# Performance work log

Hardware: AMD Instinct MI355X
Metric: run time of the kernel (lower is better)

Reference implementation:

```python
import jax, jax.numpy as jnp
import numpy as np

B, D, L = 4, 256, 4096

def setup_inputs() -> dict:
    key = jax.random.key(0)
    k1, k2, k3 = jax.random.split(key, 3)
    query = jax.random.normal(k1, (B, D, L), dtype=jnp.float32)
    context = jax.random.normal(k2, (B, D, L), dtype=jnp.float32)
    W_in = jax.random.normal(k3, (D, D), dtype=jnp.float32) * 0.02
    b_in = jnp.zeros((D,), dtype=jnp.float32)
    return {"query": query, "context": context, "W_in": W_in, "b_in": b_in}

def reference(query, context, W_in, b_in):
    # inputs are [B, D, L]; module transposes to [B, L, D]
    q = jnp.transpose(query, (0, 2, 1))    # [B, O, D]
    c = jnp.transpose(context, (0, 2, 1))  # [B, Q, D]
    # 'general': linear_in applied to query only (torch Linear: x @ W^T + b)
    q = q @ W_in.T + b_in
    # unscaled Luong attention: QK^T -> softmax -> A V
    scores = jnp.einsum('bod,bqd->boq', q, c)          # [B, O, Q]
    weights = jax.nn.softmax(scores, axis=-1)          # [B, O, Q]
    out = jnp.einsum('boq,bqd->bod', weights, c)       # [B, O, D]
    return (out, weights)
```

## Files before the change

kernel.cpp:

```cpp
#include <hip/hip_runtime.h>


#define BATCH 4
#define DDIM  256
#define LSEQ  4096
#define TQ    64

typedef float    f32x4 __attribute__((ext_vector_type(4)));
typedef _Float16 f16x8 __attribute__((ext_vector_type(8)));
typedef _Float16 f16x4 __attribute__((ext_vector_type(4)));

__device__ __forceinline__ void gld16(const void* g, void* l) {
  __builtin_amdgcn_global_load_lds((const __attribute__((address_space(1))) void*)g,
                                   (__attribute__((address_space(3))) void*)l, 16, 0, 0);
}

__global__ __launch_bounds__(256) void transpose_cast(
    const float* __restrict__ q_in, const float* __restrict__ c_in,
    _Float16* __restrict__ q_out, _Float16* __restrict__ c_out)
{
  __shared__ float tile[64][68];
  const int which = blockIdx.z >> 2;
  const int b     = blockIdx.z & 3;
  const float* __restrict__ src = which ? c_in : q_in;
  _Float16* __restrict__ dst    = which ? c_out : q_out;
  const int l0 = blockIdx.x * 64, d0 = blockIdx.y * 64;
  const int tid = threadIdx.x;
  const int tr = tid >> 4, tc = (tid & 15) << 2;
#pragma unroll
  for (int i = 0; i < 4; ++i) {
    int d = tr + i * 16;
    f32x4 v = *(const f32x4*)(src + ((size_t)b * DDIM + d0 + d) * LSEQ + l0 + tc);
    *(f32x4*)&tile[d][tc] = v;
  }
  __syncthreads();
#pragma unroll
  for (int i = 0; i < 4; ++i) {
    int l = tr + i * 16;
    f16x4 h;
    h[0] = (_Float16)tile[tc + 0][l];
    h[1] = (_Float16)tile[tc + 1][l];
    h[2] = (_Float16)tile[tc + 2][l];
    h[3] = (_Float16)tile[tc + 3][l];
    *(f16x4*)(dst + ((size_t)b * LSEQ + l0 + l) * DDIM + d0 + tc) = h;
  }
}

__global__ __launch_bounds__(256) void wconv(const float* __restrict__ w,
                                             _Float16* __restrict__ w16) {
  int i = (blockIdx.x * 256 + threadIdx.x) * 4;
  f32x4 v = *(const f32x4*)(w + i);
  f16x4 h;
  h[0] = (_Float16)v[0]; h[1] = (_Float16)v[1];
  h[2] = (_Float16)v[2]; h[3] = (_Float16)v[3];
  *(f16x4*)(w16 + i) = h;
}

__global__ __launch_bounds__(256) void castD(const float* __restrict__ c_in,
                                             _Float16* __restrict__ cD16) {
  size_t i = ((size_t)blockIdx.x * 256 + threadIdx.x) * 8;
  f32x4 a = *(const f32x4*)(c_in + i);
  f32x4 b = *(const f32x4*)(c_in + i + 4);
  f16x8 h;
  h[0] = (_Float16)a[0]; h[1] = (_Float16)a[1];
  h[2] = (_Float16)a[2]; h[3] = (_Float16)a[3];
  h[4] = (_Float16)b[0]; h[5] = (_Float16)b[1];
  h[6] = (_Float16)b[2]; h[7] = (_Float16)b[3];
  *(f16x8*)(cD16 + i) = h;
}

__global__ __launch_bounds__(256) void linear_q(
    const _Float16* __restrict__ qT16, const _Float16* __restrict__ W16,
    const float* __restrict__ bias, _Float16* __restrict__ qw16)
{
  const int tid = threadIdx.x;
  const int wv = tid >> 6, ln = tid & 63, g = ln >> 4, c16 = ln & 15;
  const size_t r0 = (size_t)blockIdx.x * 64 + wv * 16;

  f16x8 qa[8];
  const _Float16* qrow = qT16 + (r0 + c16) * DDIM + g * 8;
#pragma unroll
  for (int kk = 0; kk < 8; ++kk) qa[kk] = *(const f16x8*)(qrow + kk * 32);

  f32x4 acc[16];
#pragma unroll
  for (int n = 0; n < 16; ++n) acc[n] = f32x4{0.f, 0.f, 0.f, 0.f};

#pragma unroll 2
  for (int kk = 0; kk < 8; ++kk) {
#pragma unroll
    for (int n = 0; n < 16; ++n) {
      f16x8 bf = *(const f16x8*)(W16 + (n * 16 + c16) * DDIM + kk * 32 + g * 8);
      acc[n] = __builtin_amdgcn_mfma_f32_16x16x32_f16(qa[kk], bf, acc[n], 0, 0, 0);
    }
  }
#pragma unroll
  for (int n = 0; n < 16; ++n) {
    float bb = bias[n * 16 + c16];
#pragma unroll
    for (int r = 0; r < 4; ++r)
      qw16[(r0 + 4 * g + r) * DDIM + n * 16 + c16] = (_Float16)(acc[n][r] + bb);
  }
}

__global__ __launch_bounds__(256) void attn_main(
    const _Float16* __restrict__ qw16,
    const _Float16* __restrict__ cT16,
    const _Float16* __restrict__ cD16,
    float* __restrict__ outp,
    float* __restrict__ wgt)
{
  __shared__ __align__(16) char smem[2][65536];
  __shared__ __align__(16) char wbuf[8192];

  const int tid = threadIdx.x;
  const int wv  = tid >> 6;
  const int ln  = tid & 63;
  const int g   = ln >> 4;
  const int c16 = ln & 15;

  const int lin   = blockIdx.y * 64 + blockIdx.x;
  const int b     = (lin & 7) >> 1;
  const int otile = ((lin >> 3) << 1) | (lin & 1);
  const int o0    = otile * 64;
  const int bo    = b * LSEQ + o0;

  const _Float16* __restrict__ cbase = cT16 + (size_t)b * LSEQ * DDIM;
  const _Float16* __restrict__ cDb   = cD16 + (size_t)b * DDIM * LSEQ;

  f16x8 qa[8];
  {
    const _Float16* qrow = qw16 + ((size_t)bo + wv * 16 + c16) * DDIM + g * 8;
#pragma unroll
    for (int kk = 0; kk < 8; ++kk) qa[kk] = *(const f16x8*)(qrow + kk * 32);
  }

  auto issueA = [&](int q0s, int p) {
#pragma unroll
    for (int i = 0; i < 8; ++i) {
      unsigned x  = (unsigned)(wv * 8192 + i * 1024 + ln * 16);
      unsigned q  = x >> 9;
      unsigned db = (x & 511u) ^ ((q & 7u) << 4);
      gld16(cbase + (size_t)(q0s + q) * DDIM + (db >> 1),
            &smem[p][wv * 8192 + i * 1024]);
    }
  };
  auto issueC2 = [&](int q0s, int p) {
#pragma unroll
    for (int i = 0; i < 8; ++i) {
      unsigned x  = (unsigned)(wv * 8192 + i * 1024 + ln * 16);
      unsigned d  = x >> 7;
      unsigned qb = (x & 127u) ^ ((d & 7u) << 4);
      gld16(cDb + (size_t)d * LSEQ + q0s + (qb >> 1),
            &smem[p][32768 + wv * 8192 + i * 1024]);
    }
  };

  auto scores = [&](int p, f32x4 sa[4]) {
    const char* cl = smem[p];
#pragma unroll
    for (int qf = 0; qf < 4; ++qf) sa[qf] = f32x4{0.f, 0.f, 0.f, 0.f};
#pragma unroll
    for (int kk = 0; kk < 8; ++kk) {
#pragma unroll
      for (int qf = 0; qf < 4; ++qf) {
        unsigned off = (unsigned)(((qf * 16 + c16) * 512 + kk * 64 + g * 16)) ^
                       ((unsigned)(c16 & 7) << 4);
        f16x8 bf = *(const f16x8*)(cl + off);
        sa[qf] = __builtin_amdgcn_mfma_f32_16x16x32_f16(qa[kk], bf, sa[qf], 0, 0, 0);
      }
    }
  };

  float lsum[4] = {0.f, 0.f, 0.f, 0.f};
  int p = 0;
  issueA(0, 0);
  for (int t = 0; t < LSEQ / TQ; ++t) {
    asm volatile("s_waitcnt vmcnt(0)" ::: "memory");
    __builtin_amdgcn_s_barrier();
    if (t < LSEQ / TQ - 1) {
      issueA((t + 1) * TQ, p ^ 1);
    } else {
      issueA(0, p ^ 1);
      issueC2(0, p ^ 1);
    }
    __builtin_amdgcn_sched_barrier(0);
    f32x4 sa[4];
    scores(p, sa);
#pragma unroll
    for (int qf = 0; qf < 4; ++qf)
#pragma unroll
      for (int r = 0; r < 4; ++r) lsum[r] += __expf(sa[qf][r]);
    p ^= 1;
  }

  float invl[4];
#pragma unroll
  for (int r = 0; r < 4; ++r) {
    float v = lsum[r];
    v += __shfl_xor(v, 1);
    v += __shfl_xor(v, 2);
    v += __shfl_xor(v, 4);
    v += __shfl_xor(v, 8);
    invl[r] = 1.0f / v;
  }

  f32x4 oacc[4][4];
#pragma unroll
  for (int m = 0; m < 4; ++m)
#pragma unroll
    for (int nf = 0; nf < 4; ++nf) oacc[m][nf] = f32x4{0.f, 0.f, 0.f, 0.f};

  for (int t = 0; t < LSEQ / TQ; ++t) {
    if (t == 0) asm volatile("s_waitcnt vmcnt(0)" ::: "memory");
    else        asm volatile("s_waitcnt vmcnt(16)" ::: "memory");
    __builtin_amdgcn_s_barrier();
    if (t < LSEQ / TQ - 1) {
      issueA((t + 1) * TQ, p ^ 1);
      issueC2((t + 1) * TQ, p ^ 1);
    }
    __builtin_amdgcn_sched_barrier(0);

    const int q0 = t * TQ;
    f32x4 sa[4];
    scores(p, sa);

#pragma unroll
    for (int qf = 0; qf < 4; ++qf) {
#pragma unroll
      for (int r = 0; r < 4; ++r) {
        float w = __expf(sa[qf][r]) * invl[r];
        wgt[(size_t)(bo + wv * 16 + 4 * g + r) * LSEQ + (q0 + qf * 16 + c16)] = w;
        unsigned wb = (unsigned)((wv * 16 + 4 * g + r) * 128 + (qf * 16 + c16) * 2) ^
                      ((unsigned)((4 * g + r) & 7) << 4);
        *(_Float16*)(wbuf + wb) = (_Float16)w;
      }
    }
    asm volatile("s_waitcnt lgkmcnt(0)" ::: "memory");
    __builtin_amdgcn_s_barrier();
    __builtin_amdgcn_sched_barrier(0);

    const char* cl2 = smem[p] + 32768;
#pragma unroll
    for (int kq = 0; kq < 2; ++kq) {
      f16x8 wa[4], bv[4];
#pragma unroll
      for (int m = 0; m < 4; ++m) {
        unsigned off = (unsigned)((m * 16 + c16) * 128 + kq * 64 + g * 16) ^
                       ((unsigned)(c16 & 7) << 4);
        wa[m] = *(const f16x8*)(wbuf + off);
      }
#pragma unroll
      for (int nf = 0; nf < 4; ++nf) {
        unsigned off = (unsigned)((wv * 64 + nf * 16 + c16) * 128 + kq * 64 + g * 16) ^
                       ((unsigned)(c16 & 7) << 4);
        bv[nf] = *(const f16x8*)(cl2 + off);
      }
#pragma unroll
      for (int m = 0; m < 4; ++m)
#pragma unroll
        for (int nf = 0; nf < 4; ++nf)
          oacc[m][nf] =
              __builtin_amdgcn_mfma_f32_16x16x32_f16(wa[m], bv[nf], oacc[m][nf], 0, 0, 0);
    }
    p ^= 1;
  }

#pragma unroll
  for (int m = 0; m < 4; ++m)
#pragma unroll
    for (int nf = 0; nf < 4; ++nf)
#pragma unroll
      for (int r = 0; r < 4; ++r)
        outp[(size_t)(bo + m * 16 + 4 * g + r) * DDIM + wv * 64 + nf * 16 + c16] =
            oacc[m][nf][r];
}

extern "C" void kernel_launch(void* const* d_in, const int* in_sizes, int n_in,
                              void* d_out, int out_size, void* d_ws, size_t ws_size,
                              hipStream_t stream) {
  const float* query   = (const float*)d_in[0];
  const float* context = (const float*)d_in[1];
  const float* W_in    = (const float*)d_in[2];
  const float* b_in    = (const float*)d_in[3];

  float* outp = (float*)d_out;
  float* wgt  = outp + (size_t)BATCH * LSEQ * DDIM;

  const size_t NELEM = (size_t)BATCH * LSEQ * DDIM;
  _Float16* qT16 = (_Float16*)d_ws;
  _Float16* cT16 = qT16 + NELEM;
  _Float16* qw16 = cT16 + NELEM;
  _Float16* W16  = qw16 + NELEM;
  _Float16* cD16 = qT16;

  transpose_cast<<<dim3(LSEQ / 64, DDIM / 64, 2 * BATCH), 256, 0, stream>>>(
      query, context, qT16, cT16);
  wconv<<<(DDIM * DDIM) / 1024, 256, 0, stream>>>(W_in, W16);
  linear_q<<<(BATCH * LSEQ) / 64, 256, 0, stream>>>(qT16, W16, b_in, qw16);
  castD<<<(int)(NELEM / 2048), 256, 0, stream>>>(context, cD16);
  attn_main<<<dim3(64, BATCH), 256, 0, stream>>>(qw16, cT16, cD16, outp, wgt);
}
```

Baseline: 316.5 us.

## Split attention work across 8 waves per block with cross-wave reductions

Doubles the attn_main block to 512 threads. Each pair of waves now shares a 16-row query slice: in the score pass they split the 64-key tile into two 32-key halves, and in the A·V pass they split the K dimension. Row sums and partial output accumulators are combined through shared memory. The goal is more latency hiding and more MFMA issue parallelism, since only 256 blocks cover 256 CUs. In exchange it adds the reductions, an extra barrier, and more register pressure from the 512-thread launch bound.

```diff
diff --git a/kernel.cpp b/kernel.cpp
--- a/kernel.cpp
+++ b/kernel.cpp
@@ -103,7 +103,7 @@
   }
 }
 
-__global__ __launch_bounds__(256) void attn_main(
+__global__ __launch_bounds__(512) void attn_main(
     const _Float16* __restrict__ qw16,
     const _Float16* __restrict__ cT16,
     const _Float16* __restrict__ cD16,
@@ -112,9 +112,12 @@
 {
   __shared__ __align__(16) char smem[2][65536];
   __shared__ __align__(16) char wbuf[8192];
+  __shared__ float redbuf[2][64];
 
   const int tid = threadIdx.x;
   const int wv  = tid >> 6;
+  const int rw  = wv >> 1;
+  const int h   = wv & 1;
   const int ln  = tid & 63;
   const int g   = ln >> 4;
   const int c16 = ln & 15;
@@ -130,41 +133,41 @@
 
   f16x8 qa[8];
   {
-    const _Float16* qrow = qw16 + ((size_t)bo + wv * 16 + c16) * DDIM + g * 8;
+    const _Float16* qrow = qw16 + ((size_t)bo + rw * 16 + c16) * DDIM + g * 8;
 #pragma unroll
     for (int kk = 0; kk < 8; ++kk) qa[kk] = *(const f16x8*)(qrow + kk * 32);
   }
 
   auto issueA = [&](int q0s, int p) {
 #pragma unroll
-    for (int i = 0; i < 8; ++i) {
-      unsigned x  = (unsigned)(wv * 8192 + i * 1024 + ln * 16);
+    for (int i = 0; i < 4; ++i) {
+      unsigned x  = (unsigned)(wv * 4096 + i * 1024 + ln * 16);
       unsigned q  = x >> 9;
       unsigned db = (x & 511u) ^ ((q & 7u) << 4);
       gld16(cbase + (size_t)(q0s + q) * DDIM + (db >> 1),
-            &smem[p][wv * 8192 + i * 1024]);
+            &smem[p][wv * 4096 + i * 1024]);
     }
   };
   auto issueC2 = [&](int q0s, int p) {
 #pragma unroll
-    for (int i = 0; i < 8; ++i) {
-      unsigned x  = (unsigned)(wv * 8192 + i * 1024 + ln * 16);
+    for (int i = 0; i < 4; ++i) {
+      unsigned x  = (unsigned)(wv * 4096 + i * 1024 + ln * 16);
       unsigned d  = x >> 7;
       unsigned qb = (x & 127u) ^ ((d & 7u) << 4);
       gld16(cDb + (size_t)d * LSEQ + q0s + (qb >> 1),
-            &smem[p][32768 + wv * 8192 + i * 1024]);
+            &smem[p][32768 + wv * 4096 + i * 1024]);
     }
   };
 
-  auto scores = [&](int p, f32x4 sa[4]) {
+  auto scores = [&](int p, f32x4 sa[2]) {
     const char* cl = smem[p];
 #pragma unroll
-    for (int qf = 0; qf < 4; ++qf) sa[qf] = f32x4{0.f, 0.f, 0.f, 0.f};
+    for (int qf = 0; qf < 2; ++qf) sa[qf] = f32x4{0.f, 0.f, 0.f, 0.f};
 #pragma unroll
     for (int kk = 0; kk < 8; ++kk) {
 #pragma unroll
-      for (int qf = 0; qf < 4; ++qf) {
-        unsigned off = (unsigned)(((qf * 16 + c16) * 512 + kk * 64 + g * 16)) ^
+      for (int qf = 0; qf < 2; ++qf) {
+        unsigned off = (unsigned)(((h * 32 + qf * 16 + c16) * 512 + kk * 64 + g * 16)) ^
                        ((unsigned)(c16 & 7) << 4);
         f16x8 bf = *(const f16x8*)(cl + off);
         sa[qf] = __builtin_amdgcn_mfma_f32_16x16x32_f16(qa[kk], bf, sa[qf], 0, 0, 0);
@@ -185,16 +188,13 @@
       issueC2(0, p ^ 1);
     }
     __builtin_amdgcn_sched_barrier(0);
-    f32x4 sa[4];
+    f32x4 sa[2];
     scores(p, sa);
 #pragma unroll
-    for (int qf = 0; qf < 4; ++qf)
-#pragma unroll
-      for (int r = 0; r < 4; ++r) lsum[r] += __expf(sa[qf][r]);
+    for (int r = 0; r < 4; ++r) lsum[r] += __expf(sa[0][r]) + __expf(sa[1][r]);
     p ^= 1;
   }
 
-  float invl[4];
 #pragma unroll
   for (int r = 0; r < 4; ++r) {
     float v = lsum[r];
@@ -202,8 +202,17 @@
     v += __shfl_xor(v, 2);
     v += __shfl_xor(v, 4);
     v += __shfl_xor(v, 8);
-    invl[r] = 1.0f / v;
-  }
+    lsum[r] = v;
+  }
+  if (c16 == 0) {
+#pragma unroll
+    for (int r = 0; r < 4; ++r) redbuf[h][rw * 16 + 4 * g + r] = lsum[r];
+  }
+  __syncthreads();
+  float invl[4];
+#pragma unroll
+  for (int r = 0; r < 4; ++r)
+    invl[r] = 1.0f / (redbuf[0][rw * 16 + 4 * g + r] + redbuf[1][rw * 16 + 4 * g + r]);
 
   f32x4 oacc[4][4];
 #pragma unroll
@@ -213,7 +222,7 @@
 
   for (int t = 0; t < LSEQ / TQ; ++t) {
     if (t == 0) asm volatile("s_waitcnt vmcnt(0)" ::: "memory");
-    else        asm volatile("s_waitcnt vmcnt(16)" ::: "memory");
+    else        asm volatile("s_waitcnt vmcnt(8)" ::: "memory");
     __builtin_amdgcn_s_barrier();
     if (t < LSEQ / TQ - 1) {
       issueA((t + 1) * TQ, p ^ 1);
@@ -222,16 +231,18 @@
     __builtin_amdgcn_sched_barrier(0);
 
     const int q0 = t * TQ;
-    f32x4 sa[4];
+    f32x4 sa[2];
     scores(p, sa);
 
 #pragma unroll
-    for (int qf = 0; qf < 4; ++qf) {
+    for (int qf = 0; qf < 2; ++qf) {
 #pragma unroll
       for (int r = 0; r < 4; ++r) {
         float w = __expf(sa[qf][r]) * invl[r];
-        wgt[(size_t)(bo + wv * 16 + 4 * g + r) * LSEQ + (q0 + qf * 16 + c16)] = w;
-        unsigned wb = (unsigned)((wv * 16 + 4 * g + r) * 128 + (qf * 16 + c16) * 2) ^
+        int row = rw * 16 + 4 * g + r;
+        int col = h * 32 + qf * 16 + c16;
+        wgt[(size_t)(bo + row) * LSEQ + (q0 + col)] = w;
+        unsigned wb = (unsigned)(row * 128 + col * 2) ^
                       ((unsigned)((4 * g + r) & 7) << 4);
         *(_Float16*)(wbuf + wb) = (_Float16)w;
       }
@@ -241,18 +252,17 @@
     __builtin_amdgcn_sched_barrier(0);
 
     const char* cl2 = smem[p] + 32768;
-#pragma unroll
-    for (int kq = 0; kq < 2; ++kq) {
+    {
       f16x8 wa[4], bv[4];
 #pragma unroll
       for (int m = 0; m < 4; ++m) {
-        unsigned off = (unsigned)((m * 16 + c16) * 128 + kq * 64 + g * 16) ^
+        unsigned off = (unsigned)((m * 16 + c16) * 128 + h * 64 + g * 16) ^
                        ((unsigned)(c16 & 7) << 4);
         wa[m] = *(const f16x8*)(wbuf + off);
       }
 #pragma unroll
       for (int nf = 0; nf < 4; ++nf) {
-        unsigned off = (unsigned)((wv * 64 + nf * 16 + c16) * 128 + kq * 64 + g * 16) ^
+        unsigned off = (unsigned)((rw * 64 + nf * 16 + c16) * 128 + h * 64 + g * 16) ^
                        ((unsigned)(c16 & 7) << 4);
         bv[nf] = *(const f16x8*)(cl2 + off);
       }
@@ -266,14 +276,26 @@
     p ^= 1;
   }
 
-#pragma unroll
-  for (int m = 0; m < 4; ++m)
-#pragma unroll
-    for (int nf = 0; nf < 4; ++nf)
-#pragma unroll
-      for (int r = 0; r < 4; ++r)
-        outp[(size_t)(bo + m * 16 + 4 * g + r) * DDIM + wv * 64 + nf * 16 + c16] =
-            oacc[m][nf][r];
+  if (h == 1) {
+#pragma unroll
+    for (int m = 0; m < 4; ++m)
+#pragma unroll
+      for (int nf = 0; nf < 4; ++nf)
+        *(f32x4*)(smem[0] + rw * 16384 + (m * 4 + nf) * 1024 + ln * 16) = oacc[m][nf];
+  }
+  __syncthreads();
+  if (h == 0) {
+#pragma unroll
+    for (int m = 0; m < 4; ++m)
+#pragma unroll
+      for (int nf = 0; nf < 4; ++nf) {
+        f32x4 o2 = *(const f32x4*)(smem[0] + rw * 16384 + (m * 4 + nf) * 1024 + ln * 16);
+        f32x4 o  = oacc[m][nf] + o2;
+#pragma unroll
+        for (int r = 0; r < 4; ++r)
+          outp[(size_t)(bo + m * 16 + 4 * g + r) * DDIM + rw * 64 + nf * 16 + c16] = o[r];
+      }
+  }
 }
 
 extern "C" void kernel_launch(void* const* d_in, const int* in_sizes, int n_in,
@@ -299,5 +321,5 @@
   wconv<<<(DDIM * DDIM) / 1024, 256, 0, stream>>>(W_in, W16);
   linear_q<<<(BATCH * LSEQ) / 64, 256, 0, stream>>>(qT16, W16, b_in, qw16);
   castD<<<(int)(NELEM / 2048), 256, 0, stream>>>(context, cD16);
-  attn_main<<<dim3(64, BATCH), 256, 0, stream>>>(qw16, cT16, cD16, outp, wgt);
-}
+  attn_main<<<dim3(64, BATCH), 512, 0, stream>>>(qw16, cT16, cD16, outp, wgt);
+}
```

Result: faster. 276.8 us (-12.5%).

## Restructure attention kernel to 8 waves with split-K PV and register-fed score pass

Applied to the files above, without the earlier changes.

Doubles the block to 512 threads. Waves are now split by query slice and by output half, so each wave computes a 16x32 score tile instead of 64x16. The first (row-sum) pass loads context rows straight from global into registers with double buffering instead of staging them through LDS. The PV pass reads transposed context directly from global, splits the 64-wide q chunk across two wave groups, and reduces their partial accumulators through a 64KB LDS buffer at the end. Weight stores become 16-byte vectors. The aim is more parallelism per CU, lower LDS traffic, and better latency hiding, at the cost of more registers, an extra cross-wave reduction and a larger LDS footprint.

```diff
diff --git a/kernel.cpp b/kernel.cpp
--- a/kernel.cpp
+++ b/kernel.cpp
@@ -103,18 +103,22 @@
   }
 }
 
-__global__ __launch_bounds__(256) void attn_main(
+__global__ __launch_bounds__(512, 2) void attn_main(
     const _Float16* __restrict__ qw16,
     const _Float16* __restrict__ cT16,
     const _Float16* __restrict__ cD16,
     float* __restrict__ outp,
     float* __restrict__ wgt)
 {
-  __shared__ __align__(16) char smem[2][65536];
+  __shared__ __align__(16) char smem[2][32768];
   __shared__ __align__(16) char wbuf[8192];
+  __shared__ __align__(16) char obuf[65536];
+  __shared__ float redbuf[4][64];
 
   const int tid = threadIdx.x;
   const int wv  = tid >> 6;
+  const int qw  = wv & 3;
+  const int oh  = wv >> 2;
   const int ln  = tid & 63;
   const int g   = ln >> 4;
   const int c16 = ln & 15;
@@ -128,152 +132,157 @@
   const _Float16* __restrict__ cbase = cT16 + (size_t)b * LSEQ * DDIM;
   const _Float16* __restrict__ cDb   = cD16 + (size_t)b * DDIM * LSEQ;
 
-  f16x8 qa[8];
+  f16x8 qb[2][8];
+#pragma unroll
+  for (int of = 0; of < 2; ++of)
+#pragma unroll
+    for (int kk = 0; kk < 8; ++kk)
+      qb[of][kk] = *(const f16x8*)(qw16 +
+          ((size_t)(bo + oh * 32 + of * 16 + c16) << 8) + kk * 32 + g * 8);
+
+  float lsum0 = 0.f, lsum1 = 0.f;
+
+  auto loadA = [&](int t, f16x8 aa[8]) {
+    const _Float16* src = cbase + ((size_t)(t * TQ + qw * 16 + c16) << 8) + g * 8;
+#pragma unroll
+    for (int kk = 0; kk < 8; ++kk) aa[kk] = *(const f16x8*)(src + kk * 32);
+  };
+  auto ascore = [&](const f16x8 aa[8]) {
+    f32x4 s0{0.f, 0.f, 0.f, 0.f}, s1{0.f, 0.f, 0.f, 0.f};
+#pragma unroll
+    for (int kk = 0; kk < 8; ++kk) {
+      s0 = __builtin_amdgcn_mfma_f32_16x16x32_f16(aa[kk], qb[0][kk], s0, 0, 0, 0);
+      s1 = __builtin_amdgcn_mfma_f32_16x16x32_f16(aa[kk], qb[1][kk], s1, 0, 0, 0);
+    }
+#pragma unroll
+    for (int r = 0; r < 4; ++r) {
+      lsum0 += __expf(s0[r]);
+      lsum1 += __expf(s1[r]);
+    }
+  };
+
   {
-    const _Float16* qrow = qw16 + ((size_t)bo + wv * 16 + c16) * DDIM + g * 8;
-#pragma unroll
-    for (int kk = 0; kk < 8; ++kk) qa[kk] = *(const f16x8*)(qrow + kk * 32);
-  }
-
-  auto issueA = [&](int q0s, int p) {
-#pragma unroll
-    for (int i = 0; i < 8; ++i) {
-      unsigned x  = (unsigned)(wv * 8192 + i * 1024 + ln * 16);
+    f16x8 aaA[8], aaB[8];
+    loadA(0, aaA);
+    for (int t = 0; t < LSEQ / TQ; t += 2) {
+      loadA(t + 1, aaB);
+      ascore(aaA);
+      if (t + 2 < LSEQ / TQ) loadA(t + 2, aaA);
+      ascore(aaB);
+    }
+  }
+
+  lsum0 += __shfl_xor(lsum0, 16); lsum0 += __shfl_xor(lsum0, 32);
+  lsum1 += __shfl_xor(lsum1, 16); lsum1 += __shfl_xor(lsum1, 32);
+  if (ln < 16) {
+    redbuf[qw][oh * 32 + ln]      = lsum0;
+    redbuf[qw][oh * 32 + 16 + ln] = lsum1;
+  }
+  __syncthreads();
+  float invl[2];
+#pragma unroll
+  for (int of = 0; of < 2; ++of) {
+    int o = oh * 32 + of * 16 + c16;
+    invl[of] = 1.0f / (redbuf[0][o] + redbuf[1][o] + redbuf[2][o] + redbuf[3][o]);
+  }
+
+  auto issue_dma = [&](int t, int pp) {
+#pragma unroll
+    for (int i = 0; i < 4; ++i) {
+      unsigned x  = (unsigned)tid * 16 + i * 8192;
       unsigned q  = x >> 9;
       unsigned db = (x & 511u) ^ ((q & 7u) << 4);
-      gld16(cbase + (size_t)(q0s + q) * DDIM + (db >> 1),
-            &smem[p][wv * 8192 + i * 1024]);
+      gld16(cbase + ((size_t)(t * TQ + q) << 8) + (db >> 1), &smem[pp][x]);
     }
   };
-  auto issueC2 = [&](int q0s, int p) {
-#pragma unroll
-    for (int i = 0; i < 8; ++i) {
-      unsigned x  = (unsigned)(wv * 8192 + i * 1024 + ln * 16);
-      unsigned d  = x >> 7;
-      unsigned qb = (x & 127u) ^ ((d & 7u) << 4);
-      gld16(cDb + (size_t)d * LSEQ + q0s + (qb >> 1),
-            &smem[p][32768 + wv * 8192 + i * 1024]);
-    }
-  };
-
-  auto scores = [&](int p, f32x4 sa[4]) {
+
+  f32x4 oacc[4][4];
+#pragma unroll
+  for (int m = 0; m < 4; ++m)
+#pragma unroll
+    for (int nf = 0; nf < 4; ++nf) oacc[m][nf] = f32x4{0.f, 0.f, 0.f, 0.f};
+
+  int p = 0;
+  issue_dma(0, 0);
+  for (int t = 0; t < LSEQ / TQ; ++t) {
+    const int q0 = t * TQ;
+    if (t == 0) asm volatile("s_waitcnt vmcnt(0)" ::: "memory");
+    else        asm volatile("s_waitcnt vmcnt(2)" ::: "memory");
+    __builtin_amdgcn_s_barrier();
+    __builtin_amdgcn_sched_barrier(0);
+
+    f16x8 bv[4];
+#pragma unroll
+    for (int nf = 0; nf < 4; ++nf)
+      bv[nf] = *(const f16x8*)(cDb +
+          ((size_t)(qw * 64 + nf * 16 + c16) << 12) + q0 + oh * 32 + g * 8);
+
+    if (t < LSEQ / TQ - 1) issue_dma(t + 1, p ^ 1);
+
     const char* cl = smem[p];
-#pragma unroll
-    for (int qf = 0; qf < 4; ++qf) sa[qf] = f32x4{0.f, 0.f, 0.f, 0.f};
+    f32x4 sa0{0.f, 0.f, 0.f, 0.f}, sa1{0.f, 0.f, 0.f, 0.f};
 #pragma unroll
     for (int kk = 0; kk < 8; ++kk) {
-#pragma unroll
-      for (int qf = 0; qf < 4; ++qf) {
-        unsigned off = (unsigned)(((qf * 16 + c16) * 512 + kk * 64 + g * 16)) ^
-                       ((unsigned)(c16 & 7) << 4);
-        f16x8 bf = *(const f16x8*)(cl + off);
-        sa[qf] = __builtin_amdgcn_mfma_f32_16x16x32_f16(qa[kk], bf, sa[qf], 0, 0, 0);
+      unsigned off = (unsigned)((qw * 16 + c16) * 512 + kk * 64 + g * 16) ^
+                     ((unsigned)(c16 & 7) << 4);
+      f16x8 af = *(const f16x8*)(cl + off);
+      sa0 = __builtin_amdgcn_mfma_f32_16x16x32_f16(af, qb[0][kk], sa0, 0, 0, 0);
+      sa1 = __builtin_amdgcn_mfma_f32_16x16x32_f16(af, qb[1][kk], sa1, 0, 0, 0);
+    }
+
+#pragma unroll
+    for (int of = 0; of < 2; ++of) {
+      f32x4 sv = of ? sa1 : sa0;
+      f32x4 wv4;
+      f16x4 wh;
+#pragma unroll
+      for (int r = 0; r < 4; ++r) {
+        float w = __expf(sv[r]) * invl[of];
+        wv4[r] = w;
+        wh[r]  = (_Float16)w;
       }
-    }
-  };
-
-  float lsum[4] = {0.f, 0.f, 0.f, 0.f};
-  int p = 0;
-  issueA(0, 0);
-  for (int t = 0; t < LSEQ / TQ; ++t) {
-    asm volatile("s_waitcnt vmcnt(0)" ::: "memory");
-    __builtin_amdgcn_s_barrier();
-    if (t < LSEQ / TQ - 1) {
-      issueA((t + 1) * TQ, p ^ 1);
-    } else {
-      issueA(0, p ^ 1);
-      issueC2(0, p ^ 1);
-    }
-    __builtin_amdgcn_sched_barrier(0);
-    f32x4 sa[4];
-    scores(p, sa);
-#pragma unroll
-    for (int qf = 0; qf < 4; ++qf)
-#pragma unroll
-      for (int r = 0; r < 4; ++r) lsum[r] += __expf(sa[qf][r]);
-    p ^= 1;
-  }
-
-  float invl[4];
-#pragma unroll
-  for (int r = 0; r < 4; ++r) {
-    float v = lsum[r];
-    v += __shfl_xor(v, 1);
-    v += __shfl_xor(v, 2);
-    v += __shfl_xor(v, 4);
-    v += __shfl_xor(v, 8);
-    invl[r] = 1.0f / v;
-  }
-
-  f32x4 oacc[4][4];
-#pragma unroll
-  for (int m = 0; m < 4; ++m)
-#pragma unroll
-    for (int nf = 0; nf < 4; ++nf) oacc[m][nf] = f32x4{0.f, 0.f, 0.f, 0.f};
-
-  for (int t = 0; t < LSEQ / TQ; ++t) {
-    if (t == 0) asm volatile("s_waitcnt vmcnt(0)" ::: "memory");
-    else        asm volatile("s_waitcnt vmcnt(16)" ::: "memory");
-    __builtin_amdgcn_s_barrier();
-    if (t < LSEQ / TQ - 1) {
-      issueA((t + 1) * TQ, p ^ 1);
-      issueC2((t + 1) * TQ, p ^ 1);
-    }
-    __builtin_amdgcn_sched_barrier(0);
-
-    const int q0 = t * TQ;
-    f32x4 sa[4];
-    scores(p, sa);
-
-#pragma unroll
-    for (int qf = 0; qf < 4; ++qf) {
-#pragma unroll
-      for (int r = 0; r < 4; ++r) {
-        float w = __expf(sa[qf][r]) * invl[r];
-        wgt[(size_t)(bo + wv * 16 + 4 * g + r) * LSEQ + (q0 + qf * 16 + c16)] = w;
-        unsigned wb = (unsigned)((wv * 16 + 4 * g + r) * 128 + (qf * 16 + c16) * 2) ^
-                      ((unsigned)((4 * g + r) & 7) << 4);
-        *(_Float16*)(wbuf + wb) = (_Float16)w;
-      }
+      int o = oh * 32 + of * 16 + c16;
+      *(f32x4*)(wgt + ((size_t)(bo + o) << 12) + q0 + qw * 16 + 4 * g) = wv4;
+      unsigned wb = (unsigned)(o * 128 + qw * 32 + g * 8) ^ ((unsigned)(o & 7) << 4);
+      *(f16x4*)(wbuf + wb) = wh;
     }
     asm volatile("s_waitcnt lgkmcnt(0)" ::: "memory");
     __builtin_amdgcn_s_barrier();
     __builtin_amdgcn_sched_barrier(0);
 
-    const char* cl2 = smem[p] + 32768;
-#pragma unroll
-    for (int kq = 0; kq < 2; ++kq) {
-      f16x8 wa[4], bv[4];
-#pragma unroll
-      for (int m = 0; m < 4; ++m) {
-        unsigned off = (unsigned)((m * 16 + c16) * 128 + kq * 64 + g * 16) ^
-                       ((unsigned)(c16 & 7) << 4);
-        wa[m] = *(const f16x8*)(wbuf + off);
+#pragma unroll
+    for (int m = 0; m < 4; ++m) {
+      unsigned off = (unsigned)((m * 16 + c16) * 128 + oh * 64 + g * 16) ^
+                     ((unsigned)(c16 & 7) << 4);
+      f16x8 wa = *(const f16x8*)(wbuf + off);
+#pragma unroll
+      for (int nf = 0; nf < 4; ++nf)
+        oacc[m][nf] =
+            __builtin_amdgcn_mfma_f32_16x16x32_f16(wa, bv[nf], oacc[m][nf], 0, 0, 0);
+    }
+    p ^= 1;
+  }
+
+  if (oh == 1) {
+#pragma unroll
+    for (int m = 0; m < 4; ++m)
+#pragma unroll
+      for (int nf = 0; nf < 4; ++nf)
+        *(f32x4*)(obuf + qw * 16384 + (m * 4 + nf) * 1024 + ln * 16) = oacc[m][nf];
+  }
+  __syncthreads();
+  if (oh == 0) {
+#pragma unroll
+    for (int m = 0; m < 4; ++m)
+#pragma unroll
+      for (int nf = 0; nf < 4; ++nf) {
+        f32x4 o2 = *(const f32x4*)(obuf + qw * 16384 + (m * 4 + nf) * 1024 + ln * 16);
+        f32x4 o  = oacc[m][nf] + o2;
+#pragma unroll
+        for (int r = 0; r < 4; ++r)
+          outp[((size_t)(bo + m * 16 + 4 * g + r) << 8) + qw * 64 + nf * 16 + c16] = o[r];
       }
-#pragma unroll
-      for (int nf = 0; nf < 4; ++nf) {
-        unsigned off = (unsigned)((wv * 64 + nf * 16 + c16) * 128 + kq * 64 + g * 16) ^
-                       ((unsigned)(c16 & 7) << 4);
-        bv[nf] = *(const f16x8*)(cl2 + off);
-      }
-#pragma unroll
-      for (int m = 0; m < 4; ++m)
-#pragma unroll
-        for (int nf = 0; nf < 4; ++nf)
-          oacc[m][nf] =
-              __builtin_amdgcn_mfma_f32_16x16x32_f16(wa[m], bv[nf], oacc[m][nf], 0, 0, 0);
-    }
-    p ^= 1;
-  }
-
-#pragma unroll
-  for (int m = 0; m < 4; ++m)
-#pragma unroll
-    for (int nf = 0; nf < 4; ++nf)
-#pragma unroll
-      for (int r = 0; r < 4; ++r)
-        outp[(size_t)(bo + m * 16 + 4 * g + r) * DDIM + wv * 64 + nf * 16 + c16] =
-            oacc[m][nf][r];
+  }
 }
 
 extern "C" void kernel_launch(void* const* d_in, const int* in_sizes, int n_in,
@@ -299,5 +308,5 @@
   wconv<<<(DDIM * DDIM) / 1024, 256, 0, stream>>>(W_in, W16);
   linear_q<<<(BATCH * LSEQ) / 64, 256, 0, stream>>>(qT16, W16, b_in, qw16);
   castD<<<(int)(NELEM / 2048), 256, 0, stream>>>(context, cD16);
-  attn_main<<<dim3(64, BATCH), 256, 0, stream>>>(qw16, cT16, cD16, outp, wgt);
-}
+  attn_main<<<dim3(64, BATCH), 512, 0, stream>>>(qw16, cT16, cD16, outp, wgt);
+}
```

New measurement: 324.6 us. +2.6%, slower.
